# Kernel tuning notes

Measured on AMD Instinct MI355X. Metric: run time of the kernel, lower is better.

Reference implementation:

```python
import jax, jax.numpy as jnp
import numpy as np

B, S, H = 16, 4096, 768
NUM_WORDS = S // 2  # 2048: max distinct words per sample (padded output width)


def setup_inputs() -> dict:
    key = jax.random.key(0)
    k1, k2 = jax.random.split(key)
    hidden_states = jax.random.normal(k1, (B, S, H), dtype=jnp.float32)
    # word ids: non-decreasing, contiguous from 0; -1 marks special tokens (None in HF)
    inc = jax.random.bernoulli(k2, 0.5, (B, S)).astype(jnp.int32)
    inc = inc.at[:, :2].set(0)  # keep word 0 alive at position 1 after masking CLS
    word_ids = jnp.maximum(jnp.cumsum(inc, axis=1) - 1, 0)
    word_ids = jnp.minimum(word_ids, NUM_WORDS - 1)  # static cap on segment count
    word_ids = word_ids.at[:, 0].set(-1)   # [CLS]
    word_ids = word_ids.at[:, -1].set(-1)  # [SEP]
    return {"hidden_states": hidden_states, "word_ids": word_ids}


def reference(hidden_states, word_ids):
    # Segment-mean of subword embeddings into word embeddings.
    # hidden_states: [B, S, H] float; word_ids: [B, S] int, -1 = special token (dropped).
    b, s, h = hidden_states.shape
    valid = word_ids >= 0  # [B, S]
    # offset per-sample word ids into a flat segment space of size B*NUM_WORDS;
    # invalid tokens go to segment (b*NUM_WORDS + 0) but contribute zeros.
    wid = jnp.where(valid, word_ids, 0)
    seg = (wid + jnp.arange(b, dtype=word_ids.dtype)[:, None] * NUM_WORDS).reshape(-1)
    data = jnp.where(valid[..., None], hidden_states, 0.0).reshape(b * s, h)
    sums = jax.ops.segment_sum(data, seg, num_segments=b * NUM_WORDS)
    counts = jax.ops.segment_sum(
        valid.reshape(-1).astype(hidden_states.dtype), seg, num_segments=b * NUM_WORDS
    )
    sums = sums.reshape(b, NUM_WORDS, h)
    counts = counts.reshape(b, NUM_WORDS)
    # mean per word; words with zero tokens stay 0 (matches pad_sequence zero-padding)
    return sums / jnp.maximum(counts, 1.0)[..., None]
```

## Files before the change

### kernel.cpp

```cpp
#include <hip/hip_runtime.h>

constexpr int B = 16;
constexpr int S = 4096;
constexpr int H = 768;
constexpr int NW = 2048;
constexpr int V4 = H / 4;
constexpr int WAVES_PER_BLK = 16;

__global__ __launch_bounds__(256)
void find_starts_kernel(const int* __restrict__ wid, int* __restrict__ starts) {
    const int idx = blockIdx.x * 256 + threadIdx.x;
    const int s = idx & (S - 1);
    const int b = idx >> 12;
    if (s < 1 || s >= S - 1) return;
    const int* __restrict__ row = wid + (size_t)b * S;
    const int cur = row[s];
    if (cur != row[s - 1] && cur >= 0) starts[b * NW + cur] = s;
}

__global__ __launch_bounds__(64 * WAVES_PER_BLK)
void seg_mean_kernel(const float* __restrict__ hs,
                     const int* __restrict__ wid,
                     const int* __restrict__ starts,
                     float* __restrict__ out) {
    const int wave = threadIdx.x >> 6;
    const int lane = threadIdx.x & 63;
    const int blk = blockIdx.x * WAVES_PER_BLK + wave;
    const int b = blk >> 11;
    const int w = blk & (NW - 1);

    float4* __restrict__ o = (float4*)(out + (size_t)blk * H);

    const int maxw = wid[(size_t)b * S + (S - 2)];

    if (w > maxw) {
        float4 z = make_float4(0.f, 0.f, 0.f, 0.f);
        o[lane] = z; o[lane + 64] = z; o[lane + 128] = z;
        return;
    }

    const int start = starts[blk];
    const int end = (w == maxw) ? (S - 1) : starts[blk + 1];
    const int cnt = end - start;

    const float4* __restrict__ base = (const float4*)(hs + (size_t)b * S * H);

    float4 a0 = make_float4(0.f, 0.f, 0.f, 0.f);
    float4 a1 = a0, a2 = a0;

    int s = start;
    for (; s + 1 < end; s += 2) {
        const float4* p0 = base + (size_t)s * V4;
        const float4* p1 = p0 + V4;
        float4 v0 = p0[lane], v1 = p0[lane + 64], v2 = p0[lane + 128];
        float4 u0 = p1[lane], u1 = p1[lane + 64], u2 = p1[lane + 128];
        a0.x += v0.x; a0.y += v0.y; a0.z += v0.z; a0.w += v0.w;
        a1.x += v1.x; a1.y += v1.y; a1.z += v1.z; a1.w += v1.w;
        a2.x += v2.x; a2.y += v2.y; a2.z += v2.z; a2.w += v2.w;
        a0.x += u0.x; a0.y += u0.y; a0.z += u0.z; a0.w += u0.w;
        a1.x += u1.x; a1.y += u1.y; a1.z += u1.z; a1.w += u1.w;
        a2.x += u2.x; a2.y += u2.y; a2.z += u2.z; a2.w += u2.w;
    }
    if (s < end) {
        const float4* p0 = base + (size_t)s * V4;
        float4 v0 = p0[lane], v1 = p0[lane + 64], v2 = p0[lane + 128];
        a0.x += v0.x; a0.y += v0.y; a0.z += v0.z; a0.w += v0.w;
        a1.x += v1.x; a1.y += v1.y; a1.z += v1.z; a1.w += v1.w;
        a2.x += v2.x; a2.y += v2.y; a2.z += v2.z; a2.w += v2.w;
    }

    const float inv = 1.0f / (float)cnt;
    a0.x *= inv; a0.y *= inv; a0.z *= inv; a0.w *= inv;
    a1.x *= inv; a1.y *= inv; a1.z *= inv; a1.w *= inv;
    a2.x *= inv; a2.y *= inv; a2.z *= inv; a2.w *= inv;
    o[lane] = a0; o[lane + 64] = a1; o[lane + 128] = a2;
}

extern "C" void kernel_launch(void* const* d_in, const int* in_sizes, int n_in,
                              void* d_out, int out_size, void* d_ws, size_t ws_size,
                              hipStream_t stream) {
    const float* hs = (const float*)d_in[0];
    const int* wid = (const int*)d_in[1];
    float* out = (float*)d_out;
    int* starts = (int*)d_ws;

    find_starts_kernel<<<(B * S) / 256, 256, 0, stream>>>(wid, starts);
    seg_mean_kernel<<<(B * NW) / WAVES_PER_BLK, 64 * WAVES_PER_BLK, 0, stream>>>(
        hs, wid, starts, out);
}
```

Before: 329.9 us.

## Process eight consecutive words per wave with lane-broadcast segment bounds

Each wave now handles 8 consecutive words instead of one. The segment starts and the max word id are loaded once into separate lanes and broadcast with readlane, which replaces the per-word scalar loads. Blocks shrink from 16 waves to 4, and the grid has 8x fewer waves overall. This cuts redundant control loads and scheduling overhead, but it lowers memory-level parallelism: each wave walks its words one after another, which may leave this bandwidth-bound kernel with too few loads in flight.

Result: no change. 334.2 us (+1.3%).

```diff
diff --git a/kernel.cpp b/kernel.cpp
--- a/kernel.cpp
+++ b/kernel.cpp
@@ -5,7 +5,9 @@
 constexpr int H = 768;
 constexpr int NW = 2048;
 constexpr int V4 = H / 4;
-constexpr int WAVES_PER_BLK = 16;
+constexpr int WPW = 8;
+constexpr int WAVES_PER_BLK = 4;
+constexpr int GPS = NW / WPW;
 
 __global__ __launch_bounds__(256)
 void find_starts_kernel(const int* __restrict__ wid, int* __restrict__ starts) {
@@ -18,6 +20,10 @@
     if (cur != row[s - 1] && cur >= 0) starts[b * NW + cur] = s;
 }
 
+__device__ __forceinline__ void acc4(float4& a, const float4 v) {
+    a.x += v.x; a.y += v.y; a.z += v.z; a.w += v.w;
+}
+
 __global__ __launch_bounds__(64 * WAVES_PER_BLK)
 void seg_mean_kernel(const float* __restrict__ hs,
                      const int* __restrict__ wid,
@@ -25,55 +31,57 @@
                      float* __restrict__ out) {
     const int wave = threadIdx.x >> 6;
     const int lane = threadIdx.x & 63;
-    const int blk = blockIdx.x * WAVES_PER_BLK + wave;
-    const int b = blk >> 11;
-    const int w = blk & (NW - 1);
+    const int gw = blockIdx.x * WAVES_PER_BLK + wave;
+    const int b = gw >> 8;
+    const int w0 = (gw & (GPS - 1)) * WPW;
+    const int base_blk = b * NW + w0;
 
-    float4* __restrict__ o = (float4*)(out + (size_t)blk * H);
-
-    const int maxw = wid[(size_t)b * S + (S - 2)];
-
-    if (w > maxw) {
-        float4 z = make_float4(0.f, 0.f, 0.f, 0.f);
-        o[lane] = z; o[lane + 64] = z; o[lane + 128] = z;
-        return;
+    int ctrl;
+    if (lane <= WPW) {
+        const int i = base_blk + lane;
+        ctrl = (i < B * NW) ? starts[i] : (S - 1);
+    } else if (lane == WPW + 1) {
+        ctrl = wid[(size_t)b * S + (S - 2)];
+    } else {
+        ctrl = 0;
     }
-
-    const int start = starts[blk];
-    const int end = (w == maxw) ? (S - 1) : starts[blk + 1];
-    const int cnt = end - start;
+    const int maxw = __builtin_amdgcn_readlane(ctrl, WPW + 1);
 
     const float4* __restrict__ base = (const float4*)(hs + (size_t)b * S * H);
+    float4* __restrict__ obase = (float4*)(out + (size_t)base_blk * H);
 
-    float4 a0 = make_float4(0.f, 0.f, 0.f, 0.f);
-    float4 a1 = a0, a2 = a0;
+#pragma unroll
+    for (int i = 0; i < WPW; ++i) {
+        const int w = w0 + i;
+        const int start = __builtin_amdgcn_readlane(ctrl, i);
+        int end = (w == maxw) ? (S - 1) : __builtin_amdgcn_readlane(ctrl, i + 1);
+        if (w > maxw) end = start;
 
-    int s = start;
-    for (; s + 1 < end; s += 2) {
-        const float4* p0 = base + (size_t)s * V4;
-        const float4* p1 = p0 + V4;
-        float4 v0 = p0[lane], v1 = p0[lane + 64], v2 = p0[lane + 128];
-        float4 u0 = p1[lane], u1 = p1[lane + 64], u2 = p1[lane + 128];
-        a0.x += v0.x; a0.y += v0.y; a0.z += v0.z; a0.w += v0.w;
-        a1.x += v1.x; a1.y += v1.y; a1.z += v1.z; a1.w += v1.w;
-        a2.x += v2.x; a2.y += v2.y; a2.z += v2.z; a2.w += v2.w;
-        a0.x += u0.x; a0.y += u0.y; a0.z += u0.z; a0.w += u0.w;
-        a1.x += u1.x; a1.y += u1.y; a1.z += u1.z; a1.w += u1.w;
-        a2.x += u2.x; a2.y += u2.y; a2.z += u2.z; a2.w += u2.w;
+        float4 a0 = make_float4(0.f, 0.f, 0.f, 0.f), a1 = a0, a2 = a0;
+        int s = start;
+        for (; s + 1 < end; s += 2) {
+            const float4* p0 = base + (size_t)s * V4;
+            const float4* p1 = p0 + V4;
+            float4 v0 = p0[lane], v1 = p0[lane + 64], v2 = p0[lane + 128];
+            float4 u0 = p1[lane], u1 = p1[lane + 64], u2 = p1[lane + 128];
+            acc4(a0, v0); acc4(a1, v1); acc4(a2, v2);
+            acc4(a0, u0); acc4(a1, u1); acc4(a2, u2);
+        }
+        if (s < end) {
+            const float4* p0 = base + (size_t)s * V4;
+            float4 v0 = p0[lane], v1 = p0[lane + 64], v2 = p0[lane + 128];
+            acc4(a0, v0); acc4(a1, v1); acc4(a2, v2);
+        }
+
+        const int cnt = end - start;
+        const float inv = 1.0f / (float)(cnt > 0 ? cnt : 1);
+        a0.x *= inv; a0.y *= inv; a0.z *= inv; a0.w *= inv;
+        a1.x *= inv; a1.y *= inv; a1.z *= inv; a1.w *= inv;
+        a2.x *= inv; a2.y *= inv; a2.z *= inv; a2.w *= inv;
+
+        float4* __restrict__ o = obase + (size_t)i * V4;
+        o[lane] = a0; o[lane + 64] = a1; o[lane + 128] = a2;
     }
-    if (s < end) {
-        const float4* p0 = base + (size_t)s * V4;
-        float4 v0 = p0[lane], v1 = p0[lane + 64], v2 = p0[lane + 128];
-        a0.x += v0.x; a0.y += v0.y; a0.z += v0.z; a0.w += v0.w;
-        a1.x += v1.x; a1.y += v1.y; a1.z += v1.z; a1.w += v1.w;
-        a2.x += v2.x; a2.y += v2.y; a2.z += v2.z; a2.w += v2.w;
-    }
-
-    const float inv = 1.0f / (float)cnt;
-    a0.x *= inv; a0.y *= inv; a0.z *= inv; a0.w *= inv;
-    a1.x *= inv; a1.y *= inv; a1.z *= inv; a1.w *= inv;
-    a2.x *= inv; a2.y *= inv; a2.z *= inv; a2.w *= inv;
-    o[lane] = a0; o[lane + 64] = a1; o[lane + 128] = a2;
 }
 
 extern "C" void kernel_launch(void* const* d_in, const int* in_sizes, int n_in,
@@ -85,6 +93,6 @@
     int* starts = (int*)d_ws;
 
     find_starts_kernel<<<(B * S) / 256, 256, 0, stream>>>(wid, starts);
-    seg_mean_kernel<<<(B * NW) / WAVES_PER_BLK, 64 * WAVES_PER_BLK, 0, stream>>>(
+    seg_mean_kernel<<<(B * GPS) / WAVES_PER_BLK, 64 * WAVES_PER_BLK, 0, stream>>>(
         hs, wid, starts, out);
 }
```
